# Kernel optimization log

Hardware: AMD Instinct MI355X
Metric: run time of the kernel (lower is better)

Reference implementation:

```python
import jax, jax.numpy as jnp
import numpy as np

BLOCK = 15  # block_size from __init__
EPS = 1e-6


def setup_inputs() -> dict:
    key = jax.random.key(0)
    kq, kk, kv = jax.random.split(key, 3)
    B, H, L, D = 4, 16, 4800, 64  # L divisible by BLOCK
    return {
        "q": jax.random.normal(kq, (B, H, L, D), dtype=jnp.float32),
        "k": jax.random.normal(kk, (B, H, L, D), dtype=jnp.float32),
        "v": jax.random.normal(kv, (B, H, L, D), dtype=jnp.float32),
    }


def reference(q, k, v):
    # RobustAttention: relu(q/k/v), then independent cosFormer-style causal
    # linear attention inside each length-block of size BLOCK.
    B, H, L, D = q.shape
    w = BLOCK
    nb = L // w  # L chosen divisible; original zeros any remainder
    q = jax.nn.relu(q).reshape(B, H, nb, w, D)
    k = jax.nn.relu(k).reshape(B, H, nb, w, D)
    v = jax.nn.relu(v).reshape(B, H, nb, w, D)

    # cos_reweight index: pi/2 * (1..w) / m with m = w (block length)
    idx = (jnp.pi / 2) * jnp.arange(1, w + 1, dtype=jnp.float32) / w  # [w]
    sin = jnp.sin(idx)[:, None]  # [w,1]
    cos = jnp.cos(idx)[:, None]
    q_ = jnp.concatenate([q * sin, q * cos], axis=-1)  # [B,H,nb,w,2D]
    k_ = jnp.concatenate([k * sin, k * cos], axis=-1)

    # cumsum of outer products == causal (lower-triangular) linear attention:
    # qkv[l] = sum_{j<=l} (q_[l].k_[j]) v[j]; denom[l] = sum_{j<=l} q_[l].k_[j]
    scores = jnp.einsum('bhnqd,bhnkd->bhnqk', q_, k_)  # [B,H,nb,w,w]
    causal = jnp.tril(jnp.ones((w, w), dtype=bool))
    scores = jnp.where(causal, scores, jnp.float32(0))
    denom = jnp.maximum(scores.sum(-1), EPS)  # clamp_min(.., eps), [B,H,nb,w]
    out = jnp.einsum('bhnqk,bhnkd->bhnqd', scores, v) / denom[..., None]
    return out.reshape(B, H, L, D)
```

## Files before the change

kernel.cpp:

```cpp
#include <hip/hip_runtime.h>


namespace {

constexpr int W        = 15;
constexpr int CH       = 16;
constexpr int TILE4    = W * CH;
constexpr int TPG      = 16;
constexpr int NTHREADS = 256;
constexpr int ROWS_A   = 8;
constexpr int HALF_A4  = ROWS_A * CH;
constexpr int HALF_B4  = (W - ROWS_A) * CH;
constexpr int KSTRIDE4 = HALF_A4 + 1;

typedef float f32x4_n __attribute__((ext_vector_type(4)));

__device__ __forceinline__ float4 relu4(float4 a) {
    return make_float4(fmaxf(a.x, 0.f), fmaxf(a.y, 0.f),
                       fmaxf(a.z, 0.f), fmaxf(a.w, 0.f));
}

__global__ __launch_bounds__(NTHREADS, 2)
void robust_attn_kernel(const float4* __restrict__ q4,
                        const float4* __restrict__ k4,
                        const float4* __restrict__ v4,
                        float4* __restrict__ o4,
                        int nblocks)
{
    __shared__ float4 k_lds[TPG * KSTRIDE4];

    const int tid  = threadIdx.x;
    const int lane = tid & 15;
    const int t    = tid >> 4;
    const int g0   = blockIdx.x * TPG;
    const int g    = g0 + t;
    const bool active = (g < nblocks);
    const bool ph1    = active && (lane < W);

    {
        const size_t base = (size_t)g0 * TILE4;
#pragma unroll
        for (int r = 0; r < (TPG * HALF_A4) / NTHREADS; ++r) {
            const int idx = tid + r * NTHREADS;
            const int tt  = idx >> 7;
            const int pos = idx & 127;
            float4 kk = make_float4(0.f, 0.f, 0.f, 0.f);
            if (g0 + tt < nblocks) kk = k4[base + tt * TILE4 + pos];
            k_lds[tt * KSTRIDE4 + pos] = relu4(kk);
        }
    }
    __syncthreads();

    float s[W];
#pragma unroll
    for (int j = 0; j < W; ++j) s[j] = 0.f;

    float4 qr[CH];
    if (ph1) {
        const float4* __restrict__ qp = q4 + (size_t)g * TILE4 + lane * CH;
#pragma unroll
        for (int c = 0; c < CH; ++c) qr[c] = relu4(qp[c]);

        const float4* __restrict__ kl = &k_lds[t * KSTRIDE4];
#pragma unroll
        for (int j = 0; j < ROWS_A; ++j) {
            float acc = 0.f;
#pragma unroll
            for (int c = 0; c < CH; ++c) {
                const float4 kk = kl[j * CH + c];
                acc = fmaf(qr[c].x, kk.x, acc);
                acc = fmaf(qr[c].y, kk.y, acc);
                acc = fmaf(qr[c].z, kk.z, acc);
                acc = fmaf(qr[c].w, kk.w, acc);
            }
            s[j] = acc;
        }
    }
    __syncthreads();

    {
        const size_t base = (size_t)g0 * TILE4 + HALF_A4;
#pragma unroll
        for (int r = 0; r < (TPG * HALF_B4) / NTHREADS; ++r) {
            const int idx = tid + r * NTHREADS;
            const int tt  = idx / HALF_B4;
            const int pos = idx - tt * HALF_B4;
            float4 kk = make_float4(0.f, 0.f, 0.f, 0.f);
            if (g0 + tt < nblocks) kk = k4[base + tt * TILE4 + pos];
            k_lds[tt * KSTRIDE4 + pos] = relu4(kk);
        }
    }
    __syncthreads();

    if (ph1) {
        const int l = lane;
        const float4* __restrict__ kl = &k_lds[t * KSTRIDE4];
#pragma unroll
        for (int j = ROWS_A; j < W; ++j) {
            float acc = 0.f;
#pragma unroll
            for (int c = 0; c < CH; ++c) {
                const float4 kk = kl[(j - ROWS_A) * CH + c];
                acc = fmaf(qr[c].x, kk.x, acc);
                acc = fmaf(qr[c].y, kk.y, acc);
                acc = fmaf(qr[c].z, kk.z, acc);
                acc = fmaf(qr[c].w, kk.w, acc);
            }
            s[j] = acc;
        }

        const float step = 1.57079632679489662f / (float)W;
        float denom = 0.f;
#pragma unroll
        for (int j = 0; j < W; ++j) {
            float wc = __cosf(step * (float)(l - j));
            float tv = (j <= l) ? s[j] * wc : 0.f;
            s[j] = tv;
            denom += tv;
        }
        const float inv = 1.f / fmaxf(denom, 1e-6f);
#pragma unroll
        for (int j = 0; j < W; ++j) s[j] *= inv;
    }

    if (active) {
        const float4* __restrict__ vp = v4 + (size_t)g * TILE4 + lane;
        float4* __restrict__ op       = o4 + (size_t)g * TILE4 + lane;

        float4 vv[W];
#pragma unroll
        for (int j = 0; j < W; ++j) vv[j] = relu4(vp[j * CH]);

        const int tbase = tid & 48;
#pragma unroll
        for (int l = 0; l < W; ++l) {
            float ax = 0.f, ay = 0.f, az = 0.f, aw = 0.f;
#pragma unroll
            for (int j = 0; j <= l; ++j) {
                const float w = __shfl(s[j], tbase + l, 64);
                ax = fmaf(w, vv[j].x, ax);
                ay = fmaf(w, vv[j].y, ay);
                az = fmaf(w, vv[j].z, az);
                aw = fmaf(w, vv[j].w, aw);
            }
            f32x4_n val = {ax, ay, az, aw};
            __builtin_nontemporal_store(val, (f32x4_n*)(op + l * CH));
        }
    }
}

}

extern "C" void kernel_launch(void* const* d_in, const int* in_sizes, int n_in,
                              void* d_out, int out_size, void* d_ws, size_t ws_size,
                              hipStream_t stream) {
    const float4* q = (const float4*)d_in[0];
    const float4* k = (const float4*)d_in[1];
    const float4* v = (const float4*)d_in[2];
    float4* out = (float4*)d_out;

    const int total   = in_sizes[0];
    const int nblocks = total / (W * CH * 4);
    const int wgs     = (nblocks + TPG - 1) / TPG;

    robust_attn_kernel<<<wgs, NTHREADS, 0, stream>>>(q, k, v, out, nblocks);
}
```

Before: 76.38 us.

## Stage Q and full K tiles through padded LDS, prefetch V early

Q is now loaded with coalesced cooperative loads into a padded shared-memory tile, and each thread reads its row from there instead of issuing strided per-thread global loads. K is then staged as a whole tile in the same padded buffer, replacing the earlier two-half staging, which removes one barrier phase. V loads are issued at kernel start so their latency overlaps the Q and K staging. The cost is a larger LDS footprint (about 64 KB per workgroup) and 60 more live VGPRs held across the score phase, both of which may lower occupancy below the launch-bounds target of 2 workgroups.

```diff
diff --git a/kernel.cpp b/kernel.cpp
--- a/kernel.cpp
+++ b/kernel.cpp
@@ -8,10 +8,8 @@
 constexpr int TILE4    = W * CH;
 constexpr int TPG      = 16;
 constexpr int NTHREADS = 256;
-constexpr int ROWS_A   = 8;
-constexpr int HALF_A4  = ROWS_A * CH;
-constexpr int HALF_B4  = (W - ROWS_A) * CH;
-constexpr int KSTRIDE4 = HALF_A4 + 1;
+constexpr int RSTRIDE4 = CH + 1;
+constexpr int TSTRIDE4 = W * RSTRIDE4;
 
 typedef float f32x4_n __attribute__((ext_vector_type(4)));
 
@@ -27,7 +25,7 @@
                         float4* __restrict__ o4,
                         int nblocks)
 {
-    __shared__ float4 k_lds[TPG * KSTRIDE4];
+    __shared__ float4 lds[TPG * TSTRIDE4];
 
     const int tid  = threadIdx.x;
     const int lane = tid & 15;
@@ -37,16 +35,49 @@
     const bool active = (g < nblocks);
     const bool ph1    = active && (lane < W);
 
+    float4 vv[W];
+    if (active) {
+        const float4* __restrict__ vp = v4 + (size_t)g * TILE4 + lane;
+#pragma unroll
+        for (int j = 0; j < W; ++j) vv[j] = relu4(vp[j * CH]);
+    }
+
     {
         const size_t base = (size_t)g0 * TILE4;
 #pragma unroll
-        for (int r = 0; r < (TPG * HALF_A4) / NTHREADS; ++r) {
+        for (int r = 0; r < (TPG * TILE4) / NTHREADS; ++r) {
             const int idx = tid + r * NTHREADS;
-            const int tt  = idx >> 7;
-            const int pos = idx & 127;
-            float4 kk = make_float4(0.f, 0.f, 0.f, 0.f);
-            if (g0 + tt < nblocks) kk = k4[base + tt * TILE4 + pos];
-            k_lds[tt * KSTRIDE4 + pos] = relu4(kk);
+            const int tt  = idx / TILE4;
+            const int pos = idx - tt * TILE4;
+            const int rr  = pos >> 4;
+            const int cc  = pos & 15;
+            float4 x = make_float4(0.f, 0.f, 0.f, 0.f);
+            if (g0 + tt < nblocks) x = q4[base + idx];
+            lds[tt * TSTRIDE4 + rr * RSTRIDE4 + cc] = relu4(x);
+        }
+    }
+    __syncthreads();
+
+    float4 qr[CH];
+    if (ph1) {
+        const float4* __restrict__ ql = &lds[t * TSTRIDE4 + lane * RSTRIDE4];
+#pragma unroll
+        for (int c = 0; c < CH; ++c) qr[c] = ql[c];
+    }
+    __syncthreads();
+
+    {
+        const size_t base = (size_t)g0 * TILE4;
+#pragma unroll
+        for (int r = 0; r < (TPG * TILE4) / NTHREADS; ++r) {
+            const int idx = tid + r * NTHREADS;
+            const int tt  = idx / TILE4;
+            const int pos = idx - tt * TILE4;
+            const int rr  = pos >> 4;
+            const int cc  = pos & 15;
+            float4 x = make_float4(0.f, 0.f, 0.f, 0.f);
+            if (g0 + tt < nblocks) x = k4[base + idx];
+            lds[tt * TSTRIDE4 + rr * RSTRIDE4 + cc] = relu4(x);
         }
     }
     __syncthreads();
@@ -55,52 +86,15 @@
 #pragma unroll
     for (int j = 0; j < W; ++j) s[j] = 0.f;
 
-    float4 qr[CH];
     if (ph1) {
-        const float4* __restrict__ qp = q4 + (size_t)g * TILE4 + lane * CH;
+        const int l = lane;
+        const float4* __restrict__ kl = &lds[t * TSTRIDE4];
 #pragma unroll
-        for (int c = 0; c < CH; ++c) qr[c] = relu4(qp[c]);
-
-        const float4* __restrict__ kl = &k_lds[t * KSTRIDE4];
-#pragma unroll
-        for (int j = 0; j < ROWS_A; ++j) {
+        for (int j = 0; j < W; ++j) {
             float acc = 0.f;
 #pragma unroll
             for (int c = 0; c < CH; ++c) {
-                const float4 kk = kl[j * CH + c];
-                acc = fmaf(qr[c].x, kk.x, acc);
-                acc = fmaf(qr[c].y, kk.y, acc);
-                acc = fmaf(qr[c].z, kk.z, acc);
-                acc = fmaf(qr[c].w, kk.w, acc);
-            }
-            s[j] = acc;
-        }
-    }
-    __syncthreads();
-
-    {
-        const size_t base = (size_t)g0 * TILE4 + HALF_A4;
-#pragma unroll
-        for (int r = 0; r < (TPG * HALF_B4) / NTHREADS; ++r) {
-            const int idx = tid + r * NTHREADS;
-            const int tt  = idx / HALF_B4;
-            const int pos = idx - tt * HALF_B4;
-            float4 kk = make_float4(0.f, 0.f, 0.f, 0.f);
-            if (g0 + tt < nblocks) kk = k4[base + tt * TILE4 + pos];
-            k_lds[tt * KSTRIDE4 + pos] = relu4(kk);
-        }
-    }
-    __syncthreads();
-
-    if (ph1) {
-        const int l = lane;
-        const float4* __restrict__ kl = &k_lds[t * KSTRIDE4];
-#pragma unroll
-        for (int j = ROWS_A; j < W; ++j) {
-            float acc = 0.f;
-#pragma unroll
-            for (int c = 0; c < CH; ++c) {
-                const float4 kk = kl[(j - ROWS_A) * CH + c];
+                const float4 kk = kl[j * RSTRIDE4 + c];
                 acc = fmaf(qr[c].x, kk.x, acc);
                 acc = fmaf(qr[c].y, kk.y, acc);
                 acc = fmaf(qr[c].z, kk.z, acc);
@@ -124,12 +118,7 @@
     }
 
     if (active) {
-        const float4* __restrict__ vp = v4 + (size_t)g * TILE4 + lane;
-        float4* __restrict__ op       = o4 + (size_t)g * TILE4 + lane;
-
-        float4 vv[W];
-#pragma unroll
-        for (int j = 0; j < W; ++j) vv[j] = relu4(vp[j * CH]);
+        float4* __restrict__ op = o4 + (size_t)g * TILE4 + lane;
 
         const int tbase = tid & 48;
 #pragma unroll
```

Measured after the change: 119.2 us. +56.1%, slower.
